# Kernel tuning notes

Hardware: AMD Instinct MI355X
Metric: run time of the kernel (lower is better)

## Reference

```python
import jax, jax.numpy as jnp
import numpy as np

N_NODES = 100000
N_EDGES = 1600000
N_GRAPHS = 128
K_HOPS = 3  # TAGConv default K
HIDDEN = 128
IN_FEAT = 4
NUM_CLASSES = 2


def setup_inputs() -> dict:
    key = jax.random.key(0)
    ks = jax.random.split(key, 10)
    x = jax.random.normal(ks[0], (N_NODES, IN_FEAT), dtype=jnp.float32)
    W1 = jax.random.normal(ks[1], (K_HOPS + 1, IN_FEAT, HIDDEN), dtype=jnp.float32) * 0.1
    b1 = jax.random.normal(ks[2], (HIDDEN,), dtype=jnp.float32) * 0.1
    W2 = jax.random.normal(ks[3], (K_HOPS + 1, HIDDEN, HIDDEN), dtype=jnp.float32) * 0.1
    b2 = jax.random.normal(ks[4], (HIDDEN,), dtype=jnp.float32) * 0.1
    Wlin = jax.random.normal(ks[5], (HIDDEN, NUM_CLASSES), dtype=jnp.float32) * 0.1
    blin = jax.random.normal(ks[6], (NUM_CLASSES,), dtype=jnp.float32) * 0.1
    edge_index = jax.random.randint(ks[7], (2, N_EDGES), 0, N_NODES, dtype=jnp.int32)
    batch = jnp.sort(jax.random.randint(ks[8], (N_NODES,), 0, N_GRAPHS, dtype=jnp.int32))
    return {"x": x, "W1": W1, "b1": b1, "W2": W2, "b2": b2,
            "Wlin": Wlin, "blin": blin, "edge_index": edge_index, "batch": batch}


def _gcn_norm(edge_index, num_nodes):
    # symmetric normalization, no self-loops (TAGConv: add_self_loops=False)
    row, col = edge_index[0], edge_index[1]
    ones = jnp.ones((edge_index.shape[1],), dtype=jnp.float32)
    deg = jax.ops.segment_sum(ones, col, num_segments=num_nodes)
    dinv = jnp.where(deg > 0, jax.lax.rsqrt(jnp.maximum(deg, 1.0)), 0.0)
    return dinv[row] * dinv[col]  # [E]


def _tagconv(x, row, col, norm, W, b):
    # out = sum_k (A_norm^k x) @ W[k] + b
    out = x @ W[0]
    h = x
    for k in range(1, W.shape[0]):
        h = jax.ops.segment_sum(h[row] * norm[:, None], col, num_segments=x.shape[0])
        out = out + h @ W[k]
    return out + b


def reference(x, W1, b1, W2, b2, Wlin, blin, edge_index, batch):
    row, col = edge_index[0], edge_index[1]
    norm = _gcn_norm(edge_index, x.shape[0])
    h = jax.nn.relu(_tagconv(x, row, col, norm, W1, b1))
    h = jax.nn.relu(_tagconv(h, row, col, norm, W2, b2))
    # global mean pool over graphs
    sums = jax.ops.segment_sum(h, batch, num_segments=N_GRAPHS)
    cnts = jax.ops.segment_sum(jnp.ones((h.shape[0],), dtype=h.dtype), batch, num_segments=N_GRAPHS)
    pooled = sums / jnp.maximum(cnts, 1.0)[:, None]
    # dropout is identity in eval mode
    logits = pooled @ Wlin + blin
    return jax.nn.softmax(logits, axis=-1)
```

## Files before the change

### kernel.cpp

```cpp
#include <hip/hip_runtime.h>

#define NNODES 100000
#define NEDGES 1600000
#define NGRAPHS 128
#define HID 128
#define NBKT 782
#define CHUNK 8192
#define NCHB ((NEDGES + CHUNK - 1) / CHUNK)
#define MAXB 3072

typedef unsigned short ushort_t;
typedef unsigned int uint_t;
typedef __attribute__((ext_vector_type(8))) short short8;
typedef __attribute__((ext_vector_type(4))) float floatx4;

__device__ __forceinline__ float bf2f(ushort_t u) {
    return __uint_as_float(((unsigned)u) << 16);
}
__device__ __forceinline__ ushort_t f2bf(float f) {
    unsigned u = __float_as_uint(f);
    return (ushort_t)((u + 0x7fffu + ((u >> 16) & 1u)) >> 16);
}

__global__ void hist_k(const int* __restrict__ col, int* __restrict__ bcnt) {
    __shared__ int l[NBKT];
    for (int i = threadIdx.x; i < NBKT; i += 256) l[i] = 0;
    __syncthreads();
    int base = blockIdx.x * CHUNK;
    int lim = base + CHUNK < NEDGES ? base + CHUNK : NEDGES;
    for (int e = base + threadIdx.x; e < lim; e += 256)
        atomicAdd(&l[col[e] >> 7], 1);
    __syncthreads();
    for (int i = threadIdx.x; i < NBKT; i += 256)
        if (l[i]) atomicAdd(&bcnt[i], l[i]);
}

__global__ void bscan_k(const int* __restrict__ bcnt, int* __restrict__ bbase,
                        int* __restrict__ gc) {
    __shared__ int l[1024];
    int t = threadIdx.x;
    int v0 = (t < NBKT) ? bcnt[t] : 0;
    l[t] = v0;
    __syncthreads();
    for (int d = 1; d < 1024; d <<= 1) {
        int v = (t >= d) ? l[t - d] : 0;
        __syncthreads();
        l[t] += v;
        __syncthreads();
    }
    if (t < NBKT) { int ex = l[t] - v0; bbase[t] = ex; gc[t] = ex; }
    if (t == 0) bbase[NBKT] = NEDGES;
}

__global__ void bfill_k(const int* __restrict__ row, const int* __restrict__ col,
                        int* __restrict__ gc, uint_t* __restrict__ entry) {
    __shared__ int lcnt[NBKT], lbase[NBKT];
    for (int i = threadIdx.x; i < NBKT; i += 256) lcnt[i] = 0;
    __syncthreads();
    int base = blockIdx.x * CHUNK;
    int lim = base + CHUNK < NEDGES ? base + CHUNK : NEDGES;
    for (int e = base + threadIdx.x; e < lim; e += 256)
        atomicAdd(&lcnt[col[e] >> 7], 1);
    __syncthreads();
    for (int i = threadIdx.x; i < NBKT; i += 256) {
        int c = lcnt[i];
        lbase[i] = c ? atomicAdd(&gc[i], c) : 0;
        lcnt[i] = 0;
    }
    __syncthreads();
    for (int e = base + threadIdx.x; e < lim; e += 256) {
        int c = col[e];
        int b = c >> 7;
        int pos = lbase[b] + atomicAdd(&lcnt[b], 1);
        entry[pos] = (uint_t)row[e] | ((uint_t)(c & 127) << 17);
    }
}

__global__ void sortb_k(const uint_t* __restrict__ entry, const int* __restrict__ bbase,
                        int* __restrict__ csr_src, int* __restrict__ degi,
                        int* __restrict__ off) {
    __shared__ uint_t ents[MAXB];
    __shared__ uint_t sorted[MAXB];
    __shared__ int ncnt[128], nsc[128], nfill[128];
    int b = blockIdx.x;
    int base = bbase[b];
    int cnt = bbase[b + 1] - base;
    if (cnt > MAXB) cnt = MAXB;
    int t = threadIdx.x;
    if (t < 128) { ncnt[t] = 0; nfill[t] = 0; }
    __syncthreads();
    for (int i = t; i < cnt; i += 256) {
        uint_t v = entry[base + i];
        ents[i] = v;
        atomicAdd(&ncnt[v >> 17], 1);
    }
    __syncthreads();
    if (t < 128) nsc[t] = ncnt[t];
    __syncthreads();
    for (int d = 1; d < 128; d <<= 1) {
        int v = (t >= d && t < 128) ? nsc[t - d] : 0;
        __syncthreads();
        if (t < 128) nsc[t] += v;
        __syncthreads();
    }
    if (t < 128) {
        int n = b * 128 + t;
        if (n < NNODES) { degi[n] = ncnt[t]; off[n] = base + nsc[t]; }
        nsc[t] -= ncnt[t];
    }
    __syncthreads();
    for (int i = t; i < cnt; i += 256) {
        uint_t v = ents[i];
        int dl = v >> 17;
        int pos = nsc[dl] + atomicAdd(&nfill[dl], 1);
        sorted[pos] = v & 0x1FFFFu;
    }
    __syncthreads();
    for (int i = t; i < cnt; i += 256) csr_src[base + i] = (int)sorted[i];
}

__global__ void dinv_kernel(const int* __restrict__ degi, float* __restrict__ dinv) {
    int i = blockIdx.x * blockDim.x + threadIdx.x;
    if (i < NNODES) {
        int d = degi[i];
        dinv[i] = (d > 0) ? rsqrtf((float)d) : 0.0f;
    }
}

__global__ void gprop4(const int* __restrict__ off, const int* __restrict__ csr_src,
                       const float* __restrict__ dinv,
                       const float* __restrict__ hin, float* __restrict__ hout) {
    int n = blockIdx.x * 256 + threadIdx.x;
    if (n >= NNODES) return;
    int k = n ? off[n - 1] : 0;
    int end = off[n];
    float dn = dinv[n];
    float4 acc = {0.f, 0.f, 0.f, 0.f};
    for (; k + 3 < end; k += 4) {
        int s0 = csr_src[k], s1 = csr_src[k + 1], s2 = csr_src[k + 2], s3 = csr_src[k + 3];
        float w0 = dinv[s0] * dn, w1 = dinv[s1] * dn, w2 = dinv[s2] * dn, w3 = dinv[s3] * dn;
        float4 v0 = *(const float4*)(hin + s0 * 4);
        float4 v1 = *(const float4*)(hin + s1 * 4);
        float4 v2 = *(const float4*)(hin + s2 * 4);
        float4 v3 = *(const float4*)(hin + s3 * 4);
        acc.x += w0 * v0.x + w1 * v1.x + w2 * v2.x + w3 * v3.x;
        acc.y += w0 * v0.y + w1 * v1.y + w2 * v2.y + w3 * v3.y;
        acc.z += w0 * v0.z + w1 * v1.z + w2 * v2.z + w3 * v3.z;
        acc.w += w0 * v0.w + w1 * v1.w + w2 * v2.w + w3 * v3.w;
    }
    for (; k < end; k++) {
        int s = csr_src[k];
        float w = dinv[s] * dn;
        float4 v = *(const float4*)(hin + s * 4);
        acc.x += w * v.x; acc.y += w * v.y; acc.z += w * v.z; acc.w += w * v.w;
    }
    *(float4*)(hout + n * 4) = acc;
}

__device__ __forceinline__ void acc8(float* a, float wgt, uint4 v) {
    a[0] += wgt * __uint_as_float(v.x << 16);
    a[1] += wgt * __uint_as_float(v.x & 0xffff0000u);
    a[2] += wgt * __uint_as_float(v.y << 16);
    a[3] += wgt * __uint_as_float(v.y & 0xffff0000u);
    a[4] += wgt * __uint_as_float(v.z << 16);
    a[5] += wgt * __uint_as_float(v.z & 0xffff0000u);
    a[6] += wgt * __uint_as_float(v.w << 16);
    a[7] += wgt * __uint_as_float(v.w & 0xffff0000u);
}

__global__ void gprop128(const int* __restrict__ off, const int* __restrict__ csr_src,
                         const float* __restrict__ dinv,
                         const ushort_t* __restrict__ hin, ushort_t* __restrict__ hout) {
    int t = blockIdx.x * 256 + threadIdx.x;
    int n = t >> 4, lane = t & 15;
    if (n >= NNODES) return;
    int k = n ? off[n - 1] : 0;
    int end = off[n];
    float dn = dinv[n];
    int fo = lane * 8;
    float a[8] = {0.f, 0.f, 0.f, 0.f, 0.f, 0.f, 0.f, 0.f};
    for (; k + 3 < end; k += 4) {
        int s0 = csr_src[k], s1 = csr_src[k + 1], s2 = csr_src[k + 2], s3 = csr_src[k + 3];
        float w0 = dinv[s0] * dn, w1 = dinv[s1] * dn, w2 = dinv[s2] * dn, w3 = dinv[s3] * dn;
        uint4 v0 = *(const uint4*)(hin + s0 * HID + fo);
        uint4 v1 = *(const uint4*)(hin + s1 * HID + fo);
        uint4 v2 = *(const uint4*)(hin + s2 * HID + fo);
        uint4 v3 = *(const uint4*)(hin + s3 * HID + fo);
        acc8(a, w0, v0); acc8(a, w1, v1); acc8(a, w2, v2); acc8(a, w3, v3);
    }
    for (; k < end; k++) {
        int s = csr_src[k];
        float w = dinv[s] * dn;
        uint4 v = *(const uint4*)(hin + s * HID + fo);
        acc8(a, w, v);
    }
    uint4 o;
    o.x = (unsigned)f2bf(a[0]) | ((unsigned)f2bf(a[1]) << 16);
    o.y = (unsigned)f2bf(a[2]) | ((unsigned)f2bf(a[3]) << 16);
    o.z = (unsigned)f2bf(a[4]) | ((unsigned)f2bf(a[5]) << 16);
    o.w = (unsigned)f2bf(a[6]) | ((unsigned)f2bf(a[7]) << 16);
    *(uint4*)(hout + n * HID + fo) = o;
}

__global__ void combine1(const float* __restrict__ x, const float* __restrict__ h1,
                         const float* __restrict__ h2, const float* __restrict__ h3,
                         const float* __restrict__ W1, const float* __restrict__ b1,
                         ushort_t* __restrict__ P0) {
    __shared__ float hs[4][16];
    int n0 = blockIdx.x * 4;
    int j = threadIdx.x;
    if (j < 64) {
        int n = j >> 4, v = j & 15, k = v >> 2, i = v & 3;
        const float* src = (k == 0) ? x : (k == 1) ? h1 : (k == 2) ? h2 : h3;
        hs[n][v] = src[(n0 + n) * 4 + i];
    }
    __syncthreads();
    float w[16];
#pragma unroll
    for (int v = 0; v < 16; v++) w[v] = W1[v * 128 + j];
    float bb = b1[j];
#pragma unroll
    for (int n = 0; n < 4; n++) {
        float acc = bb;
#pragma unroll
        for (int v = 0; v < 16; v++) acc += hs[n][v] * w[v];
        P0[(n0 + n) * 128 + j] = f2bf(fmaxf(acc, 0.0f));
    }
}

__global__ void wt_kernel(const float* __restrict__ W2, ushort_t* __restrict__ Wt) {
    int t = blockIdx.x * 256 + threadIdx.x;
    if (t >= 512 * 128) return;
    int j = t >> 9, k = t & 511;
    Wt[t] = f2bf(W2[k * 128 + j]);
}

__global__ __launch_bounds__(256) void gemm4p(
    const ushort_t* __restrict__ P0, const ushort_t* __restrict__ P1,
    const ushort_t* __restrict__ P2, const ushort_t* __restrict__ P3,
    const ushort_t* __restrict__ Wt, const float* __restrict__ b2,
    const int* __restrict__ batch, float* __restrict__ sums) {
    int tid = threadIdx.x;
    int w = tid >> 6, lane = tid & 63;
    int r16 = lane & 15, kg = lane >> 4;
    int tb = (blockIdx.x * 4 + w) * 16;
    if (tb >= NNODES) return;
    int node0 = tb + r16;
    floatx4 acc[8];
#pragma unroll
    for (int n = 0; n < 8; n++) acc[n] = (floatx4){0.f, 0.f, 0.f, 0.f};
    const ushort_t* Ps[4] = {P0, P1, P2, P3};
#pragma unroll
    for (int hop = 0; hop < 4; hop++) {
        const ushort_t* P = Ps[hop];
#pragma unroll
        for (int k0 = 0; k0 < 128; k0 += 32) {
            int f = k0 + kg * 8;
            short8 a = *(const short8*)(P + node0 * HID + f);
            int kk = hop * 128 + f;
#pragma unroll
            for (int n = 0; n < 8; n++) {
                short8 b = *(const short8*)(Wt + (n * 16 + r16) * 512 + kk);
                acc[n] = __builtin_amdgcn_mfma_f32_16x16x32_bf16(a, b, acc[n], 0, 0, 0);
            }
        }
    }
    float bb[8];
#pragma unroll
    for (int n = 0; n < 8; n++) bb[n] = b2[n * 16 + r16];
    int g0 = batch[tb], g15 = batch[tb + 15];
    if (g0 == g15) {
#pragma unroll
        for (int n = 0; n < 8; n++) {
            float s = fmaxf(acc[n][0] + bb[n], 0.0f) + fmaxf(acc[n][1] + bb[n], 0.0f) +
                      fmaxf(acc[n][2] + bb[n], 0.0f) + fmaxf(acc[n][3] + bb[n], 0.0f);
            s += __shfl_xor(s, 16);
            s += __shfl_xor(s, 32);
            if (kg == 0) atomicAdd(&sums[g0 * HID + n * 16 + r16], s);
        }
    } else {
#pragma unroll
        for (int r = 0; r < 4; r++) {
            int g = batch[tb + kg * 4 + r];
#pragma unroll
            for (int n = 0; n < 8; n++)
                atomicAdd(&sums[g * HID + n * 16 + r16], fmaxf(acc[n][r] + bb[n], 0.0f));
        }
    }
}

__global__ void bounds_kernel(const int* __restrict__ batch,
                              int* __restrict__ first, int* __restrict__ last) {
    int n = blockIdx.x * 256 + threadIdx.x;
    if (n >= NNODES) return;
    int g = batch[n];
    if (n == 0 || batch[n - 1] != g) first[g] = n;
    if (n == NNODES - 1 || batch[n + 1] != g) last[g] = n;
}

__global__ void head_kernel(const float* __restrict__ sums, const int* __restrict__ first,
                            const int* __restrict__ last,
                            const float* __restrict__ Wlin, const float* __restrict__ blin,
                            float* __restrict__ out) {
    int g = threadIdx.x;
    if (g >= NGRAPHS) return;
    int f = first[g];
    float cnt = (f >= 0) ? (float)(last[g] - f + 1) : 1.0f;
    float l0 = blin[0], l1 = blin[1];
    for (int i = 0; i < HID; i++) {
        float p = sums[g * HID + i] / cnt;
        l0 += p * Wlin[i * 2 + 0];
        l1 += p * Wlin[i * 2 + 1];
    }
    float m = fmaxf(l0, l1);
    float e0 = __expf(l0 - m), e1 = __expf(l1 - m);
    float s = e0 + e1;
    out[g * 2 + 0] = e0 / s;
    out[g * 2 + 1] = e1 / s;
}

#define NPAD      100096
#define OFF_DINV  0
#define OFF_DEGI  (OFF_DINV + NPAD)
#define OFF_OFF   (OFF_DEGI + NPAD)
#define OFF_BCNT  (OFF_OFF + NPAD)
#define OFF_BBASE (OFF_BCNT + 800)
#define OFF_GC    (OFF_BBASE + 800)
#define OFF_ENT   (OFF_GC + 800)
#define OFF_SRC   (OFF_ENT + NEDGES)
#define OFF_P0    (OFF_SRC + NEDGES)
#define OFF_P1    (OFF_P0 + NNODES * HID / 2)
#define OFF_P2    (OFF_P1 + NNODES * HID / 2)
#define OFF_P3    (OFF_P2 + NNODES * HID / 2)
#define OFF_H1    (OFF_P3 + NNODES * HID / 2)
#define OFF_H2    (OFF_H1 + NNODES * 4)
#define OFF_H3    (OFF_H2 + NNODES * 4)
#define OFF_WT    (OFF_H3 + NNODES * 4)
#define OFF_SUMS  (OFF_WT + 32768)
#define OFF_FIRST (OFF_SUMS + NGRAPHS * HID)
#define OFF_LAST  (OFF_FIRST + NGRAPHS)

extern "C" void kernel_launch(void* const* d_in, const int* in_sizes, int n_in,
                              void* d_out, int out_size, void* d_ws, size_t ws_size,
                              hipStream_t stream) {
    const float* x    = (const float*)d_in[0];
    const float* W1   = (const float*)d_in[1];
    const float* b1   = (const float*)d_in[2];
    const float* W2   = (const float*)d_in[3];
    const float* b2   = (const float*)d_in[4];
    const float* Wlin = (const float*)d_in[5];
    const float* blin = (const float*)d_in[6];
    const int* ei     = (const int*)d_in[7];
    const int* batch  = (const int*)d_in[8];
    float* out = (float*)d_out;

    const int* row = ei;
    const int* col = ei + NEDGES;

    float* ws = (float*)d_ws;
    float* dinv    = ws + OFF_DINV;
    int*   degi    = (int*)(ws + OFF_DEGI);
    int*   off     = (int*)(ws + OFF_OFF);
    int*   bcnt    = (int*)(ws + OFF_BCNT);
    int*   bbase   = (int*)(ws + OFF_BBASE);
    int*   gc      = (int*)(ws + OFF_GC);
    uint_t* ent    = (uint_t*)(ws + OFF_ENT);
    int*   csr_src = (int*)(ws + OFF_SRC);
    ushort_t* P0   = (ushort_t*)(ws + OFF_P0);
    ushort_t* P1   = (ushort_t*)(ws + OFF_P1);
    ushort_t* P2   = (ushort_t*)(ws + OFF_P2);
    ushort_t* P3   = (ushort_t*)(ws + OFF_P3);
    float* h1      = ws + OFF_H1;
    float* h2      = ws + OFF_H2;
    float* h3      = ws + OFF_H3;
    ushort_t* Wt   = (ushort_t*)(ws + OFF_WT);
    float* sums    = ws + OFF_SUMS;
    int*   first   = (int*)(ws + OFF_FIRST);
    int*   last    = (int*)(ws + OFF_LAST);

    hipMemsetAsync(bcnt, 0, 800 * sizeof(int), stream);
    hipMemsetAsync(sums, 0, NGRAPHS * HID * sizeof(float), stream);
    hipMemsetAsync(first, 0xFF, 2 * NGRAPHS * sizeof(int), stream);

    hist_k<<<NCHB, 256, 0, stream>>>(col, bcnt);
    bscan_k<<<1, 1024, 0, stream>>>(bcnt, bbase, gc);
    bfill_k<<<NCHB, 256, 0, stream>>>(row, col, gc, ent);
    sortb_k<<<NBKT, 256, 0, stream>>>(ent, bbase, csr_src, degi, off);
    dinv_kernel<<<(NNODES + 255) / 256, 256, 0, stream>>>(degi, dinv);
    wt_kernel<<<(512 * 128) / 256, 256, 0, stream>>>(W2, Wt);
    bounds_kernel<<<(NNODES + 255) / 256, 256, 0, stream>>>(batch, first, last);

    gprop4<<<(NNODES + 255) / 256, 256, 0, stream>>>(off, csr_src, dinv, x, h1);
    gprop4<<<(NNODES + 255) / 256, 256, 0, stream>>>(off, csr_src, dinv, h1, h2);
    gprop4<<<(NNODES + 255) / 256, 256, 0, stream>>>(off, csr_src, dinv, h2, h3);
    combine1<<<NNODES / 4, 128, 0, stream>>>(x, h1, h2, h3, W1, b1, P0);

    gprop128<<<(NNODES * 16) / 256, 256, 0, stream>>>(off, csr_src, dinv, P0, P1);
    gprop128<<<(NNODES * 16) / 256, 256, 0, stream>>>(off, csr_src, dinv, P1, P2);
    gprop128<<<(NNODES * 16) / 256, 256, 0, stream>>>(off, csr_src, dinv, P2, P3);

    gemm4p<<<(NNODES / 16 + 3) / 4, 256, 0, stream>>>(P0, P1, P2, P3, Wt, b2, batch, sums);

    head_kernel<<<1, 128, 0, stream>>>(sums, first, last, Wlin, blin, out);
}
```

Before: 435.2 us.

## Stage weight tiles in swizzled LDS and compute two row tiles per wave in final GEMM

The final 4-hop GEMM now stages the transposed bf16 weight matrix in shared memory in two 64 KB halves, using an XOR swizzle to avoid bank conflicts. Previously every wave re-read the weights from global memory. Each wave also handles 32 nodes (two 16-row MFMA tiles), so every B fragment loaded from LDS feeds two MFMAs, and blocks cover 128 nodes. The costs are 64 KB of LDS per block, which limits occupancy, two extra block-wide barriers per stage, and more accumulator registers.

```diff
diff --git a/kernel.cpp b/kernel.cpp
--- a/kernel.cpp
+++ b/kernel.cpp
@@ -240,52 +240,78 @@
     const ushort_t* __restrict__ P2, const ushort_t* __restrict__ P3,
     const ushort_t* __restrict__ Wt, const float* __restrict__ b2,
     const int* __restrict__ batch, float* __restrict__ sums) {
+    __shared__ ushort_t Bs[32768];
     int tid = threadIdx.x;
     int w = tid >> 6, lane = tid & 63;
     int r16 = lane & 15, kg = lane >> 4;
-    int tb = (blockIdx.x * 4 + w) * 16;
-    if (tb >= NNODES) return;
-    int node0 = tb + r16;
-    floatx4 acc[8];
-#pragma unroll
-    for (int n = 0; n < 8; n++) acc[n] = (floatx4){0.f, 0.f, 0.f, 0.f};
+    int tb = blockIdx.x * 128 + w * 32;
+    bool active = (tb < NNODES);
+    floatx4 acc[2][8];
+#pragma unroll
+    for (int s = 0; s < 2; s++)
+#pragma unroll
+        for (int n = 0; n < 8; n++) acc[s][n] = (floatx4){0.f, 0.f, 0.f, 0.f};
     const ushort_t* Ps[4] = {P0, P1, P2, P3};
-#pragma unroll
-    for (int hop = 0; hop < 4; hop++) {
-        const ushort_t* P = Ps[hop];
-#pragma unroll
-        for (int k0 = 0; k0 < 128; k0 += 32) {
-            int f = k0 + kg * 8;
-            short8 a = *(const short8*)(P + node0 * HID + f);
-            int kk = hop * 128 + f;
-#pragma unroll
-            for (int n = 0; n < 8; n++) {
-                short8 b = *(const short8*)(Wt + (n * 16 + r16) * 512 + kk);
-                acc[n] = __builtin_amdgcn_mfma_f32_16x16x32_bf16(a, b, acc[n], 0, 0, 0);
+    for (int stage = 0; stage < 2; stage++) {
+        __syncthreads();
+#pragma unroll
+        for (int i = 0; i < 16; i++) {
+            int idx = i * 256 + tid;
+            int r = idx >> 5;
+            int slot = idx & 31;
+            int cb = (slot * 16) ^ ((r & 7) << 4);
+            *(uint4*)((char*)Bs + r * 512 + cb) =
+                *(const uint4*)(Wt + r * 512 + stage * 256 + slot * 8);
+        }
+        __syncthreads();
+        if (active) {
+#pragma unroll
+            for (int hh = 0; hh < 2; hh++) {
+                const ushort_t* P = Ps[stage * 2 + hh];
+#pragma unroll
+                for (int k0 = 0; k0 < 128; k0 += 32) {
+                    int f = k0 + kg * 8;
+                    short8 a0 = *(const short8*)(P + (tb + r16) * HID + f);
+                    short8 a1 = *(const short8*)(P + (tb + 16 + r16) * HID + f);
+#pragma unroll
+                    for (int n = 0; n < 8; n++) {
+                        int r = n * 16 + r16;
+                        int cb = (hh * 256 + k0 * 2 + kg * 16) ^ ((r & 7) << 4);
+                        short8 b = *(const short8*)((const char*)Bs + r * 512 + cb);
+                        acc[0][n] = __builtin_amdgcn_mfma_f32_16x16x32_bf16(a0, b, acc[0][n], 0, 0, 0);
+                        acc[1][n] = __builtin_amdgcn_mfma_f32_16x16x32_bf16(a1, b, acc[1][n], 0, 0, 0);
+                    }
+                }
             }
         }
     }
+    if (!active) return;
     float bb[8];
 #pragma unroll
     for (int n = 0; n < 8; n++) bb[n] = b2[n * 16 + r16];
-    int g0 = batch[tb], g15 = batch[tb + 15];
-    if (g0 == g15) {
+    int g0 = batch[tb], g31 = batch[tb + 31];
+    if (g0 == g31) {
 #pragma unroll
         for (int n = 0; n < 8; n++) {
-            float s = fmaxf(acc[n][0] + bb[n], 0.0f) + fmaxf(acc[n][1] + bb[n], 0.0f) +
-                      fmaxf(acc[n][2] + bb[n], 0.0f) + fmaxf(acc[n][3] + bb[n], 0.0f);
+            float s = 0.0f;
+#pragma unroll
+            for (int st = 0; st < 2; st++)
+#pragma unroll
+                for (int r = 0; r < 4; r++) s += fmaxf(acc[st][n][r] + bb[n], 0.0f);
             s += __shfl_xor(s, 16);
             s += __shfl_xor(s, 32);
             if (kg == 0) atomicAdd(&sums[g0 * HID + n * 16 + r16], s);
         }
     } else {
 #pragma unroll
-        for (int r = 0; r < 4; r++) {
-            int g = batch[tb + kg * 4 + r];
-#pragma unroll
-            for (int n = 0; n < 8; n++)
-                atomicAdd(&sums[g * HID + n * 16 + r16], fmaxf(acc[n][r] + bb[n], 0.0f));
-        }
+        for (int st = 0; st < 2; st++)
+#pragma unroll
+            for (int r = 0; r < 4; r++) {
+                int g = batch[tb + st * 16 + kg * 4 + r];
+#pragma unroll
+                for (int n = 0; n < 8; n++)
+                    atomicAdd(&sums[g * HID + n * 16 + r16], fmaxf(acc[st][n][r] + bb[n], 0.0f));
+            }
     }
 }
 
@@ -399,7 +425,7 @@
     gprop128<<<(NNODES * 16) / 256, 256, 0, stream>>>(off, csr_src, dinv, P1, P2);
     gprop128<<<(NNODES * 16) / 256, 256, 0, stream>>>(off, csr_src, dinv, P2, P3);
 
-    gemm4p<<<(NNODES / 16 + 3) / 4, 256, 0, stream>>>(P0, P1, P2, P3, Wt, b2, batch, sums);
+    gemm4p<<<(NNODES + 127) / 128, 256, 0, stream>>>(P0, P1, P2, P3, Wt, b2, batch, sums);
 
     head_kernel<<<1, 128, 0, stream>>>(sums, first, last, Wlin, blin, out);
 }
```

Result: faster. 360.1 us (-17.3%).
